# Kernel tuning notes

Measured on AMD Instinct MI355X. Metric: run time of the kernel, lower is better.

## Reference

```python
import jax, jax.numpy as jnp
import numpy as np

T = 2048; HIDDEN = 2048; HQ = 32; G = 2; D = 64
KERNEL = 32; STRIDE = 16; BLOCK = 64; TOPK = 16
INIT_BLOCKS = 1; LOCAL_BLOCKS = 2; WINDOW = 512
ROPE_BASE = 10000.0
NEG = -1e30


def _rope(x):
    # x: [T, H, D], non-interleaved rotate-half rope
    t, h, d = x.shape
    half = d // 2
    inv = 1.0 / (ROPE_BASE ** (jnp.arange(half, dtype=jnp.float32) / half))
    freqs = jnp.arange(t, dtype=jnp.float32)[:, None] * inv[None, :]
    cos = jnp.cos(freqs)[:, None, :]
    sin = jnp.sin(freqs)[:, None, :]
    x1, x2 = x[..., :half], x[..., half:]
    return jnp.concatenate([x1 * cos - x2 * sin, x2 * cos + x1 * sin], axis=-1)


def setup_inputs() -> dict:
    key = jax.random.key(0)
    ks = jax.random.split(key, 8)
    s = 0.02
    return {
        "hidden_states": jax.random.normal(ks[0], (1, T, HIDDEN), jnp.float32),
        "Wq": jax.random.normal(ks[1], (HQ * D, HIDDEN), jnp.float32) * s,
        "Wk": jax.random.normal(ks[2], (G * D, HIDDEN), jnp.float32) * s,
        "Wv": jax.random.normal(ks[3], (G * D, HIDDEN), jnp.float32) * s,
        "Wo": jax.random.normal(ks[4], (HIDDEN, HQ * D), jnp.float32) * s,
        "Wgate": jax.random.normal(ks[5], (3, HIDDEN), jnp.float32) * s,
        "compress_key": jax.random.normal(ks[6], (G, D * KERNEL, D), jnp.float32) * s,
        "compress_value": jax.random.normal(ks[7], (G, D * KERNEL, D), jnp.float32) * s,
    }


def reference(hidden_states, Wq, Wk, Wv, Wo, Wgate, compress_key, compress_value):
    x = hidden_states[0]                      # [T, HIDDEN] (single varlen sequence)
    scale = 1.0 / np.sqrt(D).astype(np.float32)
    q = (x @ Wq.T).reshape(T, HQ, D)
    k = (x @ Wk.T).reshape(T, G, D)
    v = (x @ Wv.T).reshape(T, G, D)
    gate = jax.nn.sigmoid(x @ Wgate.T)        # [T, 3]
    q = _rope(q)
    k = _rope(k)

    # --- branch 1: compressed attention (linear_compress + compressed_attention) ---
    C = (T - KERNEL) // STRIDE + 1            # compressed sequence length
    starts = jnp.arange(C) * STRIDE
    win_idx = starts[:, None] + jnp.arange(KERNEL)[None, :]        # [C, KERNEL]
    kw = k[win_idx].transpose(2, 0, 1, 3).reshape(G, C, KERNEL * D)
    vw = v[win_idx].transpose(2, 0, 1, 3).reshape(G, C, KERNEL * D)
    ck = jnp.einsum('gcf,gfd->cgd', kw, compress_key)              # [C, G, D]
    cv = jnp.einsum('gcf,gfd->cgd', vw, compress_value)

    qg = q.reshape(T, G, HQ // G, D)          # [T, G, group, D]
    cs = jnp.einsum('tghd,cgd->ghtc', qg, ck) * scale              # [G, grp, T, C]
    # query i may attend compressed token j iff i >= j*stride + kernel - 1
    cmask = jnp.arange(T)[:, None] >= (starts + KERNEL - 1)[None, :]  # [T, C]
    cs = jnp.where(cmask[None, None], cs, NEG)
    p = jax.nn.softmax(cs, axis=-1)
    valid = cmask.any(-1)                     # queries with >=1 compressed key
    p = jnp.where(valid[None, None, :, None], p, 0.0)
    comp_out = jnp.einsum('ghtc,cgd->tghd', p, cv).reshape(T, HQ, D)

    # --- topk block selection from pooled compressed attention scores ---
    NB = T // BLOCK
    bstart = jnp.arange(NB) * BLOCK
    # compressed token j overlaps key block b
    overlap = ((starts[:, None] < bstart[None, :] + BLOCK) &
               (starts[:, None] + KERNEL > bstart[None, :])).astype(p.dtype)  # [C, NB]
    score = jnp.einsum('ghtc,cb->gtb', p, overlap)                 # [G, T, NB]
    qblock = jnp.arange(T) // BLOCK
    b = jnp.arange(NB)
    causal_b = b[None, :] <= qblock[:, None]                       # [T, NB]
    forced = (b[None, :] < INIT_BLOCKS) | (((qblock[:, None] - b[None, :]) < LOCAL_BLOCKS) & causal_b)
    score = jnp.where(forced[None], jnp.inf, score)
    score = jnp.where(causal_b[None], score, -jnp.inf)
    _, topk_idx = jax.lax.top_k(score, TOPK)                       # [G, T, TOPK]
    tk_valid = jnp.take_along_axis(score, topk_idx, axis=-1) > -jnp.inf
    sel = ((topk_idx[..., None] == b) & tk_valid[..., None]).any(axis=2)  # [G, T, NB]

    # --- branch 2: topk block-sparse attention ---
    key_block = jnp.arange(T) // BLOCK
    keymask = sel[:, :, key_block]                                 # [G, T, Tk]
    causal = jnp.arange(T)[:, None] >= jnp.arange(T)[None, :]      # [T, Tk]
    smask = keymask & causal[None]
    ss = jnp.einsum('tghd,sgd->ghts', qg, k) * scale               # [G, grp, T, Tk]
    ss = jnp.where(smask[:, None], ss, NEG)
    sparse_out = jnp.einsum('ghts,sgd->tghd', jax.nn.softmax(ss, -1), v).reshape(T, HQ, D)

    # --- branch 3: sliding window attention (causal, left window) ---
    delta = jnp.arange(T)[:, None] - jnp.arange(T)[None, :]
    wmask = (delta >= 0) & (delta <= WINDOW)                       # [T, Tk]
    ws = jnp.einsum('tghd,sgd->ghts', qg, k) * scale
    ws = jnp.where(wmask[None, None], ws, NEG)
    slide_out = jnp.einsum('ghts,sgd->tghd', jax.nn.softmax(ws, -1), v).reshape(T, HQ, D)

    # --- learned gate fusion + output projection ---
    out = (gate[:, 0, None, None] * comp_out +
           gate[:, 1, None, None] * sparse_out +
           gate[:, 2, None, None] * slide_out)                    # [T, HQ, D]
    o = out.reshape(T, HQ * D) @ Wo.T
    return o[None]                                                 # [1, T, HIDDEN]
```

## Files before the change

### kernel.cpp

```cpp
#include <hip/hip_runtime.h>
#include <math.h>

#define T_SEQ 2048
#define NHQ 32
#define NG 2
#define HD 64
#define CSTRIDE 16
#define KVGW 384

typedef __attribute__((ext_vector_type(8))) short short8_t;
typedef __attribute__((ext_vector_type(4))) short short4_t;
typedef __attribute__((ext_vector_type(4))) float f32x4;

__device__ __forceinline__ ushort f2bf(float x) {
  union { float f; unsigned u; } c; c.f = x;
  unsigned r = c.u + 0x7fff + ((c.u >> 16) & 1);
  return (ushort)(r >> 16);
}
__device__ __forceinline__ float bf2f(ushort u) {
  union { unsigned u; float f; } c; c.u = ((unsigned)u) << 16;
  return c.f;
}

__device__ __forceinline__ void glds16(const ushort* g, ushort* l) {
  __builtin_amdgcn_global_load_lds(
      (const __attribute__((address_space(1))) unsigned int*)g,
      (__attribute__((address_space(3))) unsigned int*)l, 16, 0, 0);
}

__global__ __launch_bounds__(256) void mgemm(
    const ushort* __restrict__ A, const ushort* __restrict__ B,
    float* __restrict__ C, int M, int N, int K) {
  __shared__ __align__(16) ushort As[128 * 64];
  __shared__ __align__(16) ushort Bs[64 * 64];
  const int tid = threadIdx.x;
  const int lane = tid & 63, w = tid >> 6;
  const int quad = lane >> 4, l16 = lane & 15;
  const int m0 = blockIdx.y * 128, n0 = blockIdx.x * 64;
  const int mq = (w & 1) * 64, nq = (w >> 1) * 32;
  f32x4 acc[4][2];
  const f32x4 fz = {0.f, 0.f, 0.f, 0.f};
  #pragma unroll
  for (int i = 0; i < 4; ++i)
    #pragma unroll
    for (int j = 0; j < 2; ++j) acc[i][j] = fz;

  for (int k0 = 0; k0 < K; k0 += 64) {
    __syncthreads();
    #pragma unroll
    for (int j = 0; j < 4; ++j) {
      int ci = j * 256 + tid;
      int row = ci >> 3, cl = ci & 7;
      int kc = cl ^ (row & 7);
      glds16(A + ((size_t)(m0 + row) * K + k0 + kc * 8), &As[ci * 8]);
    }
    #pragma unroll
    for (int j = 0; j < 2; ++j) {
      int ci = j * 256 + tid;
      int row = ci >> 3, cl = ci & 7;
      int kc = cl ^ (row & 7);
      glds16(B + ((size_t)(n0 + row) * K + k0 + kc * 8), &Bs[ci * 8]);
    }
    __syncthreads();
    #pragma unroll
    for (int kt = 0; kt < 2; ++kt) {
      short8_t af[4], bf_[2];
      #pragma unroll
      for (int mt = 0; mt < 4; ++mt) {
        int row = mq + mt * 16 + l16;
        int cl = (kt * 4 + quad) ^ (row & 7);
        af[mt] = *(const short8_t*)&As[row * 64 + cl * 8];
      }
      #pragma unroll
      for (int nt = 0; nt < 2; ++nt) {
        int row = nq + nt * 16 + l16;
        int cl = (kt * 4 + quad) ^ (row & 7);
        bf_[nt] = *(const short8_t*)&Bs[row * 64 + cl * 8];
      }
      #pragma unroll
      for (int mt = 0; mt < 4; ++mt)
        #pragma unroll
        for (int nt = 0; nt < 2; ++nt)
          acc[mt][nt] = __builtin_amdgcn_mfma_f32_16x16x32_bf16(
              af[mt], bf_[nt], acc[mt][nt], 0, 0, 0);
    }
  }
  #pragma unroll
  for (int mt = 0; mt < 4; ++mt)
    #pragma unroll
    for (int nt = 0; nt < 2; ++nt)
      #pragma unroll
      for (int r = 0; r < 4; ++r) {
        int m = m0 + mq + mt * 16 + quad * 4 + r;
        int n = n0 + nq + nt * 16 + l16;
        C[(size_t)m * N + n] = acc[mt][nt][r];
      }
}

__global__ __launch_bounds__(256) void cvt_bf(const float* __restrict__ src,
                                              ushort* __restrict__ dst, int n) {
  int i = (blockIdx.x * 256 + threadIdx.x) * 4;
  if (i >= n) return;
  float4 v = *(const float4*)(src + i);
  short4_t o = {(short)f2bf(v.x), (short)f2bf(v.y),
                (short)f2bf(v.z), (short)f2bf(v.w)};
  *(short4_t*)(dst + i) = o;
}

__global__ __launch_bounds__(256) void cvt_sum2_bf(const float* __restrict__ a,
                                                   const float* __restrict__ b,
                                                   ushort* __restrict__ dst, int n) {
  int i = (blockIdx.x * 256 + threadIdx.x) * 4;
  if (i >= n) return;
  float4 va = *(const float4*)(a + i);
  float4 vb = *(const float4*)(b + i);
  short4_t o = {(short)f2bf(va.x + vb.x), (short)f2bf(va.y + vb.y),
                (short)f2bf(va.z + vb.z), (short)f2bf(va.w + vb.w)};
  *(short4_t*)(dst + i) = o;
}

__global__ __launch_bounds__(256) void pack_wkvg(
    const float* __restrict__ Wk, const float* __restrict__ Wv,
    const float* __restrict__ Wg, ushort* __restrict__ dst) {
  int i = blockIdx.x * 256 + threadIdx.x;
  if (i >= KVGW * 2048) return;
  int n = i >> 11, k = i & 2047;
  float v;
  if (n < 128) v = Wk[(size_t)n * 2048 + k];
  else if (n < 256) v = Wv[(size_t)(n - 128) * 2048 + k];
  else if (n < 259) v = Wg[(size_t)(n - 256) * 2048 + k];
  else v = 0.f;
  dst[i] = f2bf(v);
}

__global__ __launch_bounds__(256) void cvt_vt(const float* __restrict__ kvg,
                                              ushort* __restrict__ vt) {
  int i = blockIdx.x * 256 + threadIdx.x;
  if (i >= T_SEQ * NG * HD) return;
  int d = i & 63, g = (i >> 6) & 1, s = i >> 7;
  int blk = s >> 6, k = s & 63;
  int snew = blk * 64 + (((k >> 2) ^ (d & 15)) << 2) + (k & 3);
  vt[((size_t)g * HD + d) * T_SEQ + snew] =
      f2bf(kvg[(size_t)s * KVGW + 128 + g * 64 + d]);
}

__global__ __launch_bounds__(256) void rope_all(
    const float* __restrict__ q, float* __restrict__ kvg,
    ushort* __restrict__ qbf, ushort* __restrict__ kbf) {
  const int t = blockIdx.x;
  const float lnb_over = 9.210340371976184f / 32.f;
  for (int job = threadIdx.x; job < (NHQ + NG) * 32; job += 256) {
    int h = job >> 5, j = job & 31;
    float inv = expf(-(float)j * lnb_over);
    float fr = (float)t * inv;
    float c_ = cosf(fr), s_ = sinf(fr);
    if (h < NHQ) {
      const float cq = c_ * 0.125f, sq = s_ * 0.125f;
      const float* base = q + ((size_t)t * NHQ + h) * HD;
      float x1 = base[j], x2 = base[j + 32];
      ushort* ob = qbf + ((size_t)t * NHQ + h) * HD;
      ob[j] = f2bf(x1 * cq - x2 * sq);
      ob[j + 32] = f2bf(x2 * cq + x1 * sq);
    } else {
      int g = h - NHQ;
      float* base = kvg + (size_t)t * KVGW + g * 64;
      float x1 = base[j], x2 = base[j + 32];
      float o1 = x1 * c_ - x2 * s_, o2 = x2 * c_ + x1 * s_;
      base[j] = o1; base[j + 32] = o2;
      kbf[(size_t)t * 128 + g * 64 + j] = f2bf(o1);
      kbf[(size_t)t * 128 + g * 64 + j + 32] = f2bf(o2);
    }
  }
}

__global__ __launch_bounds__(256) void compress_kv(
    const float* __restrict__ kvg,
    const float* __restrict__ Wck, const float* __restrict__ Wcv,
    ushort* __restrict__ ck16, ushort* __restrict__ cvt16) {
  const int c = blockIdx.x, g = blockIdx.y;
  const int tid = threadIdx.x;
  if (c == 127) {
    if (tid < 64) ck16[((size_t)127 * NG + g) * HD + tid] = 0;
    else if (tid < 128) cvt16[((size_t)g * HD + (tid - 64)) * 128 + 127] = 0;
    return;
  }
  const int d = tid & 63, chunk = tid >> 6;
  __shared__ float red[2][4][64];
  float ak = 0.f, av = 0.f;
  for (int f = chunk * 512; f < chunk * 512 + 512; ++f) {
    int i = f >> 6, e = f & 63;
    int trow = c * CSTRIDE + i;
    float kv = kvg[(size_t)trow * KVGW + g * 64 + e];
    float vv = kvg[(size_t)trow * KVGW + 128 + g * 64 + e];
    ak += kv * Wck[((size_t)g * 2048 + f) * HD + d];
    av += vv * Wcv[((size_t)g * 2048 + f) * HD + d];
  }
  red[0][chunk][d] = ak;
  red[1][chunk][d] = av;
  __syncthreads();
  if (tid < 64) {
    ck16[((size_t)c * NG + g) * HD + tid] =
        f2bf(red[0][0][tid] + red[0][1][tid] + red[0][2][tid] + red[0][3][tid]);
  } else if (tid < 128) {
    int dd = tid - 64;
    cvt16[((size_t)g * HD + dd) * 128 + c] =
        f2bf(red[1][0][dd] + red[1][1][dd] + red[1][2][dd] + red[1][3][dd]);
  }
}

__global__ __launch_bounds__(512) void comp_attn(
    const ushort* __restrict__ qbf, const ushort* __restrict__ ck16,
    const ushort* __restrict__ cvt16, const float* __restrict__ kvg,
    float* __restrict__ comb, unsigned* __restrict__ sel) {
  const int tb = 127 - blockIdx.x, g = blockIdx.y;
  const int t0 = tb * 16;
  const int tid = threadIdx.x, lane = tid & 63, w = tid >> 6;
  const int quad = lane >> 4, l16 = lane & 15;
  const int qb = t0 >> 6;

  __shared__ float colsum[16][129];
  for (int i = tid; i < 16 * 129; i += 512) ((float*)colsum)[i] = 0.f;
  __syncthreads();

  const int t = t0 + l16;
  const int cmaxv = (t >= 31) ? min(126, (t - 31) >> 4) : -1;
  const int h0 = w * 2;

  short8_t qB[2][2];
  #pragma unroll
  for (int hh = 0; hh < 2; ++hh)
    #pragma unroll
    for (int kd = 0; kd < 2; ++kd)
      qB[hh][kd] = *(const short8_t*)(qbf +
          ((size_t)t * NHQ + g * 16 + h0 + hh) * HD + kd * 32 + quad * 8);

  const f32x4 fz = {0.f, 0.f, 0.f, 0.f};
  f32x4 sp[2][8];

  #pragma unroll
  for (int ct = 0; ct < 8; ++ct) {
    const ushort* kr = ck16 + ((size_t)(ct * 16 + l16) * NG + g) * HD + quad * 8;
    short8_t kA0 = *(const short8_t*)kr;
    short8_t kA1 = *(const short8_t*)(kr + 32);
    #pragma unroll
    for (int hh = 0; hh < 2; ++hh) {
      f32x4 c0 = __builtin_amdgcn_mfma_f32_16x16x32_bf16(kA0, qB[hh][0], fz, 0, 0, 0);
      sp[hh][ct] = __builtin_amdgcn_mfma_f32_16x16x32_bf16(kA1, qB[hh][1], c0, 0, 0, 0);
    }
  }

  short4_t pB[2][8];
  #pragma unroll
  for (int hh = 0; hh < 2; ++hh) {
    float mx = -INFINITY;
    #pragma unroll
    for (int ct = 0; ct < 8; ++ct)
      #pragma unroll
      for (int r = 0; r < 4; ++r) {
        int c = ct * 16 + quad * 4 + r;
        float s_ = (c <= cmaxv) ? sp[hh][ct][r] : -INFINITY;
        sp[hh][ct][r] = s_;
        mx = fmaxf(mx, s_);
      }
    mx = fmaxf(mx, __shfl_xor(mx, 16));
    mx = fmaxf(mx, __shfl_xor(mx, 32));
    if (mx == -INFINITY) mx = 0.f;
    float ls = 0.f;
    #pragma unroll
    for (int ct = 0; ct < 8; ++ct)
      #pragma unroll
      for (int r = 0; r < 4; ++r) {
        float p = __expf(sp[hh][ct][r] - mx);
        sp[hh][ct][r] = p;
        ls += p;
      }
    ls += __shfl_xor(ls, 16);
    ls += __shfl_xor(ls, 32);
    float inv = (ls > 0.f) ? 1.f / ls : 0.f;
    #pragma unroll
    for (int ct = 0; ct < 8; ++ct) {
      short4_t pk;
      #pragma unroll
      for (int r = 0; r < 4; ++r) {
        float pn = sp[hh][ct][r] * inv;
        sp[hh][ct][r] = pn;
        pk[r] = (short)f2bf(pn);
      }
      pB[hh][ct] = pk;
    }
  }

  #pragma unroll
  for (int ct = 0; ct < 8; ++ct)
    #pragma unroll
    for (int r = 0; r < 4; ++r)
      atomicAdd(&colsum[l16][ct * 16 + quad * 4 + r],
                sp[0][ct][r] + sp[1][ct][r]);

  f32x4 acc[2][4];
  #pragma unroll
  for (int hh = 0; hh < 2; ++hh)
    #pragma unroll
    for (int dt = 0; dt < 4; ++dt) acc[hh][dt] = fz;
  #pragma unroll
  for (int ct = 0; ct < 8; ++ct) {
    short4_t vA[4];
    #pragma unroll
    for (int dt = 0; dt < 4; ++dt)
      vA[dt] = *(const short4_t*)(cvt16 +
          ((size_t)g * HD + dt * 16 + l16) * 128 + ct * 16 + quad * 4);
    #pragma unroll
    for (int hh = 0; hh < 2; ++hh)
      #pragma unroll
      for (int dt = 0; dt < 4; ++dt)
        acc[hh][dt] = __builtin_amdgcn_mfma_f32_16x16x16bf16_1k(
            vA[dt], pB[hh][ct], acc[hh][dt], 0, 0, 0);
  }

  const float g0 = 1.f / (1.f + __expf(-kvg[(size_t)t * KVGW + 256]));
  #pragma unroll
  for (int hh = 0; hh < 2; ++hh)
    #pragma unroll
    for (int dt = 0; dt < 4; ++dt)
      #pragma unroll
      for (int r = 0; r < 4; ++r)
        comb[((size_t)t * NHQ + g * 16 + h0 + hh) * HD + dt * 16 + quad * 4 + r] =
            g0 * acc[hh][dt][r];

  __syncthreads();

  {
    const int tl = tid >> 5;
    const int b = tid & 31;
    float s;
    if (b > qb) s = -INFINITY;
    else if (b == 0 || qb - b < 2) s = INFINITY;
    else {
      s = 0.f;
      #pragma unroll
      for (int i = 0; i < 5; ++i) s += colsum[tl][4 * b - 1 + i];
    }
    unsigned key = (s < 0.f) ? 0u : (__float_as_uint(s) + 1u);
    unsigned msel = 0;
    for (int it = 0; it < 16; ++it) {
      unsigned long long pk =
          (((unsigned long long)key) << 6) | (unsigned)(63 - b);
      #pragma unroll
      for (int off = 16; off >= 1; off >>= 1) {
        unsigned long long o = __shfl_xor(pk, off);
        if (o > pk) pk = o;
      }
      if ((pk >> 6) == 0) break;
      int bs = 63 - (int)(pk & 63);
      msel |= 1u << bs;
      if (b == bs) key = 0;
    }
    if (b == 0) sel[(size_t)(t0 + tl) * NG + g] = msel;
  }
}

__global__ __launch_bounds__(512, 2) void mfma_attn(
    const ushort* __restrict__ qb16, const ushort* __restrict__ kb16,
    const ushort* __restrict__ vtb, const float* __restrict__ kvg,
    const unsigned* __restrict__ sel, float* __restrict__ comb1,
    float* __restrict__ comb2) {
  const int qb = 31 - blockIdx.x, g = blockIdx.y;
  const int hgp = blockIdx.z & 7, mode = blockIdx.z >> 3;
  const int tid = threadIdx.x, lane = tid & 63, w = tid >> 6;
  const int quad = lane >> 4, l16 = lane & 15;
  const int head = g * 16 + hgp * 2 + (w >> 2);
  const int t0 = qb * 64;

  __shared__ __align__(16) ushort Ks[2][64 * 64];
  __shared__ __align__(16) ushort Vs[2][64 * 64];
  __shared__ unsigned sel_s[64];

  if (tid < 64) sel_s[tid] = sel[(size_t)(t0 + tid) * NG + g];
  __syncthreads();

  const int qg = t0 + (w & 3) * 16 + l16;
  const unsigned sbq = sel_s[(w & 3) * 16 + l16];

  short8_t qB0 = *(const short8_t*)(qb16 +
      ((size_t)qg * NHQ + head) * HD + quad * 8);
  short8_t qB1 = *(const short8_t*)(qb16 +
      ((size_t)qg * NHQ + head) * HD + 32 + quad * 8);

  float m_ = -1e30f;
  f32x4 acc[4], accL;
  const f32x4 fz = {0.f, 0.f, 0.f, 0.f};
  #pragma unroll
  for (int dt = 0; dt < 4; ++dt) acc[dt] = fz;
  accL = fz;
  const short4_t onesA = {(short)0x3F80, (short)0x3F80,
                          (short)0x3F80, (short)0x3F80};

  unsigned mrem = 0; int b0 = 0, nb = 0;
  if (mode == 0) {
    unsigned uni = sel_s[lane];
    #pragma unroll
    for (int off = 32; off >= 1; off >>= 1) uni |= __shfl_xor(uni, off);
    mrem = uni;
    nb = __popc(mrem);
  } else {
    b0 = (qb > 8) ? qb - 8 : 0;
    nb = qb - b0 + 1;
  }

  #define STAGE(buf, blk)                                                     \
    {                                                                         \
      const int blk_ = (blk);                                                 \
      const int row = tid >> 3, cl = tid & 7;                                 \
      const int kck = cl ^ (row & 7);                                         \
      glds16(kb16 + (size_t)(blk_ * 64 + row) * 128 + g * 64 + kck * 8,       \
             &Ks[buf][tid * 8]);                                              \
      glds16(vtb + ((size_t)g * 64 + row) * 2048 + blk_ * 64 + cl * 8,        \
             &Vs[buf][tid * 8]);                                              \
    }

  int blkcur;
  if (mode == 0) { blkcur = __ffs(mrem) - 1; mrem &= mrem - 1; }
  else blkcur = b0;
  STAGE(0, blkcur);
  __syncthreads();

  const int e = l16 & 7;

  for (int ib = 0; ib < nb; ++ib) {
    const int cur = ib & 1;
    const int blk = blkcur;
    if (ib + 1 < nb) {
      if (mode == 0) { blkcur = __ffs(mrem) - 1; mrem &= mrem - 1; }
      else blkcur = b0 + ib + 1;
      STAGE(cur ^ 1, blkcur);
    }

    f32x4 sp[4];
    __builtin_amdgcn_s_setprio(1);
    #pragma unroll
    for (int kt = 0; kt < 4; ++kt) {
      const ushort* kr = &Ks[cur][(kt * 16 + l16) * 64];
      short8_t kA0 = *(const short8_t*)(kr + ((quad ^ e) * 8));
      short8_t kA1 = *(const short8_t*)(kr + ((quad ^ e ^ 4) * 8));
      f32x4 c = __builtin_amdgcn_mfma_f32_16x16x32_bf16(kA0, qB0, fz, 0, 0, 0);
      sp[kt] = __builtin_amdgcn_mfma_f32_16x16x32_bf16(kA1, qB1, c, 0, 0, 0);
    }
    __builtin_amdgcn_s_setprio(0);

    const bool diag = (blk == qb);
    const bool wedge = (mode == 1) && (blk == qb - 8);
    const bool selq = (mode != 0) || (((sbq >> blk) & 1u) != 0);

    float mx = -INFINITY;
    if (!diag && !wedge) {
      #pragma unroll
      for (int kt = 0; kt < 4; ++kt)
        #pragma unroll
        for (int r = 0; r < 4; ++r) {
          float s_ = selq ? sp[kt][r] : -INFINITY;
          sp[kt][r] = s_;
          mx = fmaxf(mx, s_);
        }
    } else {
      #pragma unroll
      for (int kt = 0; kt < 4; ++kt)
        #pragma unroll
        for (int r = 0; r < 4; ++r) {
          int key = blk * 64 + kt * 16 + quad * 4 + r;
          bool ok = selq && (key <= qg) && (qg - key <= 512);
          float s_ = ok ? sp[kt][r] : -INFINITY;
          sp[kt][r] = s_;
          mx = fmaxf(mx, s_);
        }
    }
    mx = fmaxf(mx, __shfl_xor(mx, 16));
    mx = fmaxf(mx, __shfl_xor(mx, 32));
    float mold = m_;
    if (!__all(mx <= mold + 8.f)) {
      float mnew = fmaxf(mold, mx);
      float alpha = __expf(mold - mnew);
      #pragma unroll
      for (int dt = 0; dt < 4; ++dt)
        #pragma unroll
        for (int r = 0; r < 4; ++r) acc[dt][r] *= alpha;
      #pragma unroll
      for (int r = 0; r < 4; ++r) accL[r] *= alpha;
      m_ = mnew;
      mold = mnew;
    }
    short4_t pB[4];
    #pragma unroll
    for (int kt = 0; kt < 4; ++kt) {
      float p0 = __expf(sp[kt][0] - mold);
      float p1 = __expf(sp[kt][1] - mold);
      float p2 = __expf(sp[kt][2] - mold);
      float p3 = __expf(sp[kt][3] - mold);
      union { unsigned u[2]; short4_t s; } pk;
      asm("v_cvt_pk_bf16_f32 %0, %1, %2" : "=v"(pk.u[0]) : "v"(p0), "v"(p1));
      asm("v_cvt_pk_bf16_f32 %0, %1, %2" : "=v"(pk.u[1]) : "v"(p2), "v"(p3));
      pB[kt] = pk.s;
    }

    __builtin_amdgcn_s_setprio(1);
    #pragma unroll
    for (int kt = 0; kt < 4; ++kt) {
      #pragma unroll
      for (int dt = 0; dt < 4; ++dt) {
        short4_t vA = *(const short4_t*)(&Vs[cur][(dt * 16 + l16) * 64 +
                                                  (((kt * 4 + quad) ^ l16) << 2)]);
        acc[dt] = __builtin_amdgcn_mfma_f32_16x16x16bf16_1k(
            vA, pB[kt], acc[dt], 0, 0, 0);
      }
      accL = __builtin_amdgcn_mfma_f32_16x16x16bf16_1k(
          onesA, pB[kt], accL, 0, 0, 0);
    }
    __builtin_amdgcn_s_setprio(0);

    __syncthreads();
  }
  #undef STAGE

  const float l_ = accL[0];
  const float c_ =
      (1.f / (1.f + __expf(-kvg[(size_t)qg * KVGW + 257 + mode]))) / l_;
  #pragma unroll
  for (int dt = 0; dt < 4; ++dt)
    #pragma unroll
    for (int r = 0; r < 4; ++r) {
      const int d = dt * 16 + quad * 4 + r;
      size_t idx = ((size_t)qg * NHQ + head) * HD + d;
      if (mode == 0) comb1[idx] += c_ * acc[dt][r];
      else           comb2[idx]  = c_ * acc[dt][r];
    }
}

extern "C" void kernel_launch(void* const* d_in, const int* in_sizes, int n_in,
                              void* d_out, int out_size, void* d_ws, size_t ws_size,
                              hipStream_t stream) {
  const float* x   = (const float*)d_in[0];
  const float* Wq  = (const float*)d_in[1];
  const float* Wk  = (const float*)d_in[2];
  const float* Wv  = (const float*)d_in[3];
  const float* Wo  = (const float*)d_in[4];
  const float* Wg  = (const float*)d_in[5];
  const float* Wck = (const float*)d_in[6];
  const float* Wcv = (const float*)d_in[7];
  float* out = (float*)d_out;
  float* ws = (float*)d_ws;

  float* qbuf   = ws;
  float* comb1  = qbuf + 4194304;
  float* kvg    = comb1 + 4194304;
  float* ckb    = kvg + 786432;
  float* cvb    = ckb + 16384;
  unsigned* sel = (unsigned*)(cvb + 16384);
  ushort* kbf   = (ushort*)(sel + 4096);
  ushort* vtb   = kbf + 262144;
  ushort* wkvgb = vtb + 262144;
  ushort* regA  = wkvgb + 786432;
  ushort* regB  = regA + 4194304;
  ushort* xb = regA;      ushort* combb = regA;
  ushort* wqb = regB;     ushort* qbf = regB;
  float* comb2 = qbuf;
  ushort* wob = (ushort*)qbuf;

  ushort* ckb16 = (ushort*)ckb;
  ushort* cvtb  = ckb16 + 16384;

  const int CV4 = (1048576 + 255) / 256;
  cvt_bf<<<CV4, 256, 0, stream>>>(x, xb, 4194304);
  cvt_bf<<<CV4, 256, 0, stream>>>(Wq, wqb, 4194304);
  pack_wkvg<<<(KVGW * 2048 + 255) / 256, 256, 0, stream>>>(Wk, Wv, Wg, wkvgb);

  mgemm<<<dim3(32, 16), 256, 0, stream>>>(xb, wqb, qbuf, 2048, 2048, 2048);
  mgemm<<<dim3(6, 16), 256, 0, stream>>>(xb, wkvgb, kvg, 2048, KVGW, 2048);

  rope_all<<<2048, 256, 0, stream>>>(qbuf, kvg, qbf, kbf);
  cvt_vt<<<(262144 + 255) / 256, 256, 0, stream>>>(kvg, vtb);
  compress_kv<<<dim3(128, 2), 256, 0, stream>>>(kvg, Wck, Wcv, ckb16, cvtb);
  comp_attn<<<dim3(128, 2), 512, 0, stream>>>(qbf, ckb16, cvtb, kvg, comb1, sel);
  mfma_attn<<<dim3(32, 2, 16), 512, 0, stream>>>(qbf, kbf, vtb, kvg, sel, comb1, comb2);

  cvt_sum2_bf<<<CV4, 256, 0, stream>>>(comb1, comb2, combb, 4194304);
  cvt_bf<<<CV4, 256, 0, stream>>>(Wo, wob, 4194304);
  mgemm<<<dim3(32, 16), 256, 0, stream>>>(combb, wob, out, 2048, 2048, 2048);
}
```

Baseline: 388.1 us.

## Fuse sparse and sliding-window attention passes; batch compress_kv over eight windows

The attention kernel now handles the selected-block and sliding-window branches in one pass. It iterates over the union of both block sets, so each K/V tile is staged and the QK^T product computed once, with separate online-softmax accumulators for the two branches and the gated results summed in registers. This removes the second launch dimension, the duplicate K/V loads, and the read-modify-write of comb1. compress_kv now computes eight compressed windows per block to reuse the compression-weight loads, at the cost of fewer blocks and more registers. The fused kernel holds two sets of accumulators, which raises register pressure and may hurt occupancy.

```diff
diff --git a/kernel.cpp b/kernel.cpp
--- a/kernel.cpp
+++ b/kernel.cpp
@@ -177,34 +177,49 @@
     const float* __restrict__ kvg,
     const float* __restrict__ Wck, const float* __restrict__ Wcv,
     ushort* __restrict__ ck16, ushort* __restrict__ cvt16) {
-  const int c = blockIdx.x, g = blockIdx.y;
+  const int c0 = blockIdx.x * 8, g = blockIdx.y;
   const int tid = threadIdx.x;
-  if (c == 127) {
-    if (tid < 64) ck16[((size_t)127 * NG + g) * HD + tid] = 0;
-    else if (tid < 128) cvt16[((size_t)g * HD + (tid - 64)) * 128 + 127] = 0;
-    return;
-  }
   const int d = tid & 63, chunk = tid >> 6;
-  __shared__ float red[2][4][64];
-  float ak = 0.f, av = 0.f;
+  __shared__ float red[2][8][4][64];
+  float ak[8], av[8];
+  #pragma unroll
+  for (int cc = 0; cc < 8; ++cc) { ak[cc] = 0.f; av[cc] = 0.f; }
   for (int f = chunk * 512; f < chunk * 512 + 512; ++f) {
     int i = f >> 6, e = f & 63;
-    int trow = c * CSTRIDE + i;
-    float kv = kvg[(size_t)trow * KVGW + g * 64 + e];
-    float vv = kvg[(size_t)trow * KVGW + 128 + g * 64 + e];
-    ak += kv * Wck[((size_t)g * 2048 + f) * HD + d];
-    av += vv * Wcv[((size_t)g * 2048 + f) * HD + d];
-  }
-  red[0][chunk][d] = ak;
-  red[1][chunk][d] = av;
+    float wck = Wck[((size_t)g * 2048 + f) * HD + d];
+    float wcv = Wcv[((size_t)g * 2048 + f) * HD + d];
+    #pragma unroll
+    for (int cc = 0; cc < 8; ++cc) {
+      int trow = (c0 + cc) * CSTRIDE + i;
+      if (trow < T_SEQ) {
+        ak[cc] += kvg[(size_t)trow * KVGW + g * 64 + e] * wck;
+        av[cc] += kvg[(size_t)trow * KVGW + 128 + g * 64 + e] * wcv;
+      }
+    }
+  }
+  #pragma unroll
+  for (int cc = 0; cc < 8; ++cc) {
+    red[0][cc][chunk][d] = ak[cc];
+    red[1][cc][chunk][d] = av[cc];
+  }
   __syncthreads();
   if (tid < 64) {
-    ck16[((size_t)c * NG + g) * HD + tid] =
-        f2bf(red[0][0][tid] + red[0][1][tid] + red[0][2][tid] + red[0][3][tid]);
+    #pragma unroll
+    for (int cc = 0; cc < 8; ++cc) {
+      int c = c0 + cc;
+      float s = red[0][cc][0][tid] + red[0][cc][1][tid] +
+                red[0][cc][2][tid] + red[0][cc][3][tid];
+      ck16[((size_t)c * NG + g) * HD + tid] = (c == 127) ? (ushort)0 : f2bf(s);
+    }
   } else if (tid < 128) {
     int dd = tid - 64;
-    cvt16[((size_t)g * HD + dd) * 128 + c] =
-        f2bf(red[1][0][dd] + red[1][1][dd] + red[1][2][dd] + red[1][3][dd]);
+    #pragma unroll
+    for (int cc = 0; cc < 8; ++cc) {
+      int c = c0 + cc;
+      float s = red[1][cc][0][dd] + red[1][cc][1][dd] +
+                red[1][cc][2][dd] + red[1][cc][3][dd];
+      cvt16[((size_t)g * HD + dd) * 128 + c] = (c == 127) ? (ushort)0 : f2bf(s);
+    }
   }
 }
 
@@ -362,10 +377,9 @@
 __global__ __launch_bounds__(512, 2) void mfma_attn(
     const ushort* __restrict__ qb16, const ushort* __restrict__ kb16,
     const ushort* __restrict__ vtb, const float* __restrict__ kvg,
-    const unsigned* __restrict__ sel, float* __restrict__ comb1,
-    float* __restrict__ comb2) {
+    const unsigned* __restrict__ sel, float* __restrict__ comb2) {
   const int qb = 31 - blockIdx.x, g = blockIdx.y;
-  const int hgp = blockIdx.z & 7, mode = blockIdx.z >> 3;
+  const int hgp = blockIdx.z;
   const int tid = threadIdx.x, lane = tid & 63, w = tid >> 6;
   const int quad = lane >> 4, l16 = lane & 15;
   const int head = g * 16 + hgp * 2 + (w >> 2);
@@ -386,26 +400,22 @@
   short8_t qB1 = *(const short8_t*)(qb16 +
       ((size_t)qg * NHQ + head) * HD + 32 + quad * 8);
 
-  float m_ = -1e30f;
-  f32x4 acc[4], accL;
+  float m0 = -1e30f, m1 = -1e30f;
+  f32x4 acc0[4], acc1[4], accL0, accL1;
   const f32x4 fz = {0.f, 0.f, 0.f, 0.f};
   #pragma unroll
-  for (int dt = 0; dt < 4; ++dt) acc[dt] = fz;
-  accL = fz;
+  for (int dt = 0; dt < 4; ++dt) { acc0[dt] = fz; acc1[dt] = fz; }
+  accL0 = fz; accL1 = fz;
   const short4_t onesA = {(short)0x3F80, (short)0x3F80,
                           (short)0x3F80, (short)0x3F80};
 
-  unsigned mrem = 0; int b0 = 0, nb = 0;
-  if (mode == 0) {
-    unsigned uni = sel_s[lane];
-    #pragma unroll
-    for (int off = 32; off >= 1; off >>= 1) uni |= __shfl_xor(uni, off);
-    mrem = uni;
-    nb = __popc(mrem);
-  } else {
-    b0 = (qb > 8) ? qb - 8 : 0;
-    nb = qb - b0 + 1;
-  }
+  unsigned uni = sel_s[lane];
+  #pragma unroll
+  for (int off = 32; off >= 1; off >>= 1) uni |= __shfl_xor(uni, off);
+  const int b0w = (qb > 8) ? qb - 8 : 0;
+  const unsigned wmask = ((1u << (qb - b0w + 1)) - 1u) << b0w;
+  unsigned lrem = uni | wmask;
+  const int nb = __popc(lrem);
 
   #define STAGE(buf, blk)                                                     \
     {                                                                         \
@@ -418,9 +428,7 @@
              &Vs[buf][tid * 8]);                                              \
     }
 
-  int blkcur;
-  if (mode == 0) { blkcur = __ffs(mrem) - 1; mrem &= mrem - 1; }
-  else blkcur = b0;
+  int blkcur = __ffs(lrem) - 1; lrem &= lrem - 1;
   STAGE(0, blkcur);
   __syncthreads();
 
@@ -430,8 +438,7 @@
     const int cur = ib & 1;
     const int blk = blkcur;
     if (ib + 1 < nb) {
-      if (mode == 0) { blkcur = __ffs(mrem) - 1; mrem &= mrem - 1; }
-      else blkcur = b0 + ib + 1;
+      blkcur = __ffs(lrem) - 1; lrem &= lrem - 1;
       STAGE(cur ^ 1, blkcur);
     }
 
@@ -448,89 +455,168 @@
     __builtin_amdgcn_s_setprio(0);
 
     const bool diag = (blk == qb);
-    const bool wedge = (mode == 1) && (blk == qb - 8);
-    const bool selq = (mode != 0) || (((sbq >> blk) & 1u) != 0);
-
-    float mx = -INFINITY;
-    if (!diag && !wedge) {
-      #pragma unroll
-      for (int kt = 0; kt < 4; ++kt)
-        #pragma unroll
-        for (int r = 0; r < 4; ++r) {
-          float s_ = selq ? sp[kt][r] : -INFINITY;
-          sp[kt][r] = s_;
-          mx = fmaxf(mx, s_);
+    const bool wedge = (blk == qb - 8);
+    const bool inU = ((uni >> blk) & 1u) != 0;
+    const bool inW = ((wmask >> blk) & 1u) != 0;
+    const bool selq = ((sbq >> blk) & 1u) != 0;
+
+    float rm = -INFINITY;
+    #pragma unroll
+    for (int kt = 0; kt < 4; ++kt)
+      #pragma unroll
+      for (int r = 0; r < 4; ++r) rm = fmaxf(rm, sp[kt][r]);
+    rm = fmaxf(rm, __shfl_xor(rm, 16));
+    rm = fmaxf(rm, __shfl_xor(rm, 32));
+
+    if (inU) {
+      float mx;
+      if (!diag) {
+        mx = selq ? rm : -INFINITY;
+      } else {
+        mx = -INFINITY;
+        #pragma unroll
+        for (int kt = 0; kt < 4; ++kt)
+          #pragma unroll
+          for (int r = 0; r < 4; ++r) {
+            int key = blk * 64 + kt * 16 + quad * 4 + r;
+            bool ok = selq && (key <= qg);
+            mx = ok ? fmaxf(mx, sp[kt][r]) : mx;
+          }
+        mx = fmaxf(mx, __shfl_xor(mx, 16));
+        mx = fmaxf(mx, __shfl_xor(mx, 32));
+      }
+      if (!__all(mx <= m0 + 8.f)) {
+        float mnew = fmaxf(m0, mx);
+        float alpha = __expf(m0 - mnew);
+        #pragma unroll
+        for (int dt = 0; dt < 4; ++dt)
+          #pragma unroll
+          for (int r = 0; r < 4; ++r) acc0[dt][r] *= alpha;
+        #pragma unroll
+        for (int r = 0; r < 4; ++r) accL0[r] *= alpha;
+        m0 = mnew;
+      }
+      short4_t pB[4];
+      #pragma unroll
+      for (int kt = 0; kt < 4; ++kt) {
+        union { unsigned u[2]; short4_t s; } pk;
+        if (!diag) {
+          float p0 = __expf(sp[kt][0] - m0), p1 = __expf(sp[kt][1] - m0);
+          float p2 = __expf(sp[kt][2] - m0), p3 = __expf(sp[kt][3] - m0);
+          asm("v_cvt_pk_bf16_f32 %0, %1, %2" : "=v"(pk.u[0]) : "v"(p0), "v"(p1));
+          asm("v_cvt_pk_bf16_f32 %0, %1, %2" : "=v"(pk.u[1]) : "v"(p2), "v"(p3));
+          pk.u[0] = selq ? pk.u[0] : 0u;
+          pk.u[1] = selq ? pk.u[1] : 0u;
+        } else {
+          float p[4];
+          #pragma unroll
+          for (int r = 0; r < 4; ++r) {
+            int key = blk * 64 + kt * 16 + quad * 4 + r;
+            bool ok = selq && (key <= qg);
+            p[r] = ok ? __expf(sp[kt][r] - m0) : 0.f;
+          }
+          asm("v_cvt_pk_bf16_f32 %0, %1, %2" : "=v"(pk.u[0]) : "v"(p[0]), "v"(p[1]));
+          asm("v_cvt_pk_bf16_f32 %0, %1, %2" : "=v"(pk.u[1]) : "v"(p[2]), "v"(p[3]));
         }
-    } else {
-      #pragma unroll
-      for (int kt = 0; kt < 4; ++kt)
-        #pragma unroll
-        for (int r = 0; r < 4; ++r) {
-          int key = blk * 64 + kt * 16 + quad * 4 + r;
-          bool ok = selq && (key <= qg) && (qg - key <= 512);
-          float s_ = ok ? sp[kt][r] : -INFINITY;
-          sp[kt][r] = s_;
-          mx = fmaxf(mx, s_);
+        pB[kt] = pk.s;
+      }
+      __builtin_amdgcn_s_setprio(1);
+      #pragma unroll
+      for (int kt = 0; kt < 4; ++kt) {
+        #pragma unroll
+        for (int dt = 0; dt < 4; ++dt) {
+          short4_t vA = *(const short4_t*)(&Vs[cur][(dt * 16 + l16) * 64 +
+                                                    (((kt * 4 + quad) ^ l16) << 2)]);
+          acc0[dt] = __builtin_amdgcn_mfma_f32_16x16x16bf16_1k(
+              vA, pB[kt], acc0[dt], 0, 0, 0);
         }
-    }
-    mx = fmaxf(mx, __shfl_xor(mx, 16));
-    mx = fmaxf(mx, __shfl_xor(mx, 32));
-    float mold = m_;
-    if (!__all(mx <= mold + 8.f)) {
-      float mnew = fmaxf(mold, mx);
-      float alpha = __expf(mold - mnew);
-      #pragma unroll
-      for (int dt = 0; dt < 4; ++dt)
-        #pragma unroll
-        for (int r = 0; r < 4; ++r) acc[dt][r] *= alpha;
-      #pragma unroll
-      for (int r = 0; r < 4; ++r) accL[r] *= alpha;
-      m_ = mnew;
-      mold = mnew;
-    }
-    short4_t pB[4];
-    #pragma unroll
-    for (int kt = 0; kt < 4; ++kt) {
-      float p0 = __expf(sp[kt][0] - mold);
-      float p1 = __expf(sp[kt][1] - mold);
-      float p2 = __expf(sp[kt][2] - mold);
-      float p3 = __expf(sp[kt][3] - mold);
-      union { unsigned u[2]; short4_t s; } pk;
-      asm("v_cvt_pk_bf16_f32 %0, %1, %2" : "=v"(pk.u[0]) : "v"(p0), "v"(p1));
-      asm("v_cvt_pk_bf16_f32 %0, %1, %2" : "=v"(pk.u[1]) : "v"(p2), "v"(p3));
-      pB[kt] = pk.s;
-    }
-
-    __builtin_amdgcn_s_setprio(1);
-    #pragma unroll
-    for (int kt = 0; kt < 4; ++kt) {
-      #pragma unroll
-      for (int dt = 0; dt < 4; ++dt) {
-        short4_t vA = *(const short4_t*)(&Vs[cur][(dt * 16 + l16) * 64 +
-                                                  (((kt * 4 + quad) ^ l16) << 2)]);
-        acc[dt] = __builtin_amdgcn_mfma_f32_16x16x16bf16_1k(
-            vA, pB[kt], acc[dt], 0, 0, 0);
-      }
-      accL = __builtin_amdgcn_mfma_f32_16x16x16bf16_1k(
-          onesA, pB[kt], accL, 0, 0, 0);
-    }
-    __builtin_amdgcn_s_setprio(0);
+        accL0 = __builtin_amdgcn_mfma_f32_16x16x16bf16_1k(
+            onesA, pB[kt], accL0, 0, 0, 0);
+      }
+      __builtin_amdgcn_s_setprio(0);
+    }
+
+    if (inW) {
+      float mx;
+      if (!diag && !wedge) {
+        mx = rm;
+      } else {
+        mx = -INFINITY;
+        #pragma unroll
+        for (int kt = 0; kt < 4; ++kt)
+          #pragma unroll
+          for (int r = 0; r < 4; ++r) {
+            int key = blk * 64 + kt * 16 + quad * 4 + r;
+            bool ok = (key <= qg) && (qg - key <= 512);
+            mx = ok ? fmaxf(mx, sp[kt][r]) : mx;
+          }
+        mx = fmaxf(mx, __shfl_xor(mx, 16));
+        mx = fmaxf(mx, __shfl_xor(mx, 32));
+      }
+      if (!__all(mx <= m1 + 8.f)) {
+        float mnew = fmaxf(m1, mx);
+        float alpha = __expf(m1 - mnew);
+        #pragma unroll
+        for (int dt = 0; dt < 4; ++dt)
+          #pragma unroll
+          for (int r = 0; r < 4; ++r) acc1[dt][r] *= alpha;
+        #pragma unroll
+        for (int r = 0; r < 4; ++r) accL1[r] *= alpha;
+        m1 = mnew;
+      }
+      short4_t pB[4];
+      #pragma unroll
+      for (int kt = 0; kt < 4; ++kt) {
+        union { unsigned u[2]; short4_t s; } pk;
+        if (!diag && !wedge) {
+          float p0 = __expf(sp[kt][0] - m1), p1 = __expf(sp[kt][1] - m1);
+          float p2 = __expf(sp[kt][2] - m1), p3 = __expf(sp[kt][3] - m1);
+          asm("v_cvt_pk_bf16_f32 %0, %1, %2" : "=v"(pk.u[0]) : "v"(p0), "v"(p1));
+          asm("v_cvt_pk_bf16_f32 %0, %1, %2" : "=v"(pk.u[1]) : "v"(p2), "v"(p3));
+        } else {
+          float p[4];
+          #pragma unroll
+          for (int r = 0; r < 4; ++r) {
+            int key = blk * 64 + kt * 16 + quad * 4 + r;
+            bool ok = (key <= qg) && (qg - key <= 512);
+            p[r] = ok ? __expf(sp[kt][r] - m1) : 0.f;
+          }
+          asm("v_cvt_pk_bf16_f32 %0, %1, %2" : "=v"(pk.u[0]) : "v"(p[0]), "v"(p[1]));
+          asm("v_cvt_pk_bf16_f32 %0, %1, %2" : "=v"(pk.u[1]) : "v"(p[2]), "v"(p[3]));
+        }
+        pB[kt] = pk.s;
+      }
+      __builtin_amdgcn_s_setprio(1);
+      #pragma unroll
+      for (int kt = 0; kt < 4; ++kt) {
+        #pragma unroll
+        for (int dt = 0; dt < 4; ++dt) {
+          short4_t vA = *(const short4_t*)(&Vs[cur][(dt * 16 + l16) * 64 +
+                                                    (((kt * 4 + quad) ^ l16) << 2)]);
+          acc1[dt] = __builtin_amdgcn_mfma_f32_16x16x16bf16_1k(
+              vA, pB[kt], acc1[dt], 0, 0, 0);
+        }
+        accL1 = __builtin_amdgcn_mfma_f32_16x16x16bf16_1k(
+            onesA, pB[kt], accL1, 0, 0, 0);
+      }
+      __builtin_amdgcn_s_setprio(0);
+    }
 
     __syncthreads();
   }
   #undef STAGE
 
-  const float l_ = accL[0];
-  const float c_ =
-      (1.f / (1.f + __expf(-kvg[(size_t)qg * KVGW + 257 + mode]))) / l_;
+  const float c0 =
+      (1.f / (1.f + __expf(-kvg[(size_t)qg * KVGW + 257]))) / accL0[0];
+  const float c1 =
+      (1.f / (1.f + __expf(-kvg[(size_t)qg * KVGW + 258]))) / accL1[0];
   #pragma unroll
   for (int dt = 0; dt < 4; ++dt)
     #pragma unroll
     for (int r = 0; r < 4; ++r) {
       const int d = dt * 16 + quad * 4 + r;
-      size_t idx = ((size_t)qg * NHQ + head) * HD + d;
-      if (mode == 0) comb1[idx] += c_ * acc[dt][r];
-      else           comb2[idx]  = c_ * acc[dt][r];
+      comb2[((size_t)qg * NHQ + head) * HD + d] =
+          c0 * acc0[dt][r] + c1 * acc1[dt][r];
     }
 }
 
@@ -577,9 +663,9 @@
 
   rope_all<<<2048, 256, 0, stream>>>(qbuf, kvg, qbf, kbf);
   cvt_vt<<<(262144 + 255) / 256, 256, 0, stream>>>(kvg, vtb);
-  compress_kv<<<dim3(128, 2), 256, 0, stream>>>(kvg, Wck, Wcv, ckb16, cvtb);
+  compress_kv<<<dim3(16, 2), 256, 0, stream>>>(kvg, Wck, Wcv, ckb16, cvtb);
   comp_attn<<<dim3(128, 2), 512, 0, stream>>>(qbf, ckb16, cvtb, kvg, comb1, sel);
-  mfma_attn<<<dim3(32, 2, 16), 512, 0, stream>>>(qbf, kbf, vtb, kvg, sel, comb1, comb2);
+  mfma_attn<<<dim3(32, 2, 8), 512, 0, stream>>>(qbf, kbf, vtb, kvg, sel, comb2);
 
   cvt_sum2_bf<<<CV4, 256, 0, stream>>>(comb1, comb2, combb, 4194304);
   cvt_bf<<<CV4, 256, 0, stream>>>(Wo, wob, 4194304);
```

New measurement: 867.0 us. 123% more time.
